# Performance work log

Measured on AMD Instinct MI355X. Metric: run time of the kernel, lower is better.

The kernel has to match this reference:

```python
import jax, jax.numpy as jnp
import numpy as np

N_NODES = 50000
N_EDGES = 800000
D_IN = 128
HC = 128
D_OUT = 128
BN_EPS = 1e-5
RRELU_SLOPE = (1.0 / 8.0 + 1.0 / 3.0) / 2.0  # RReLU eval mode: (lower+upper)/2 = 11/48


def setup_inputs() -> dict:
    key = jax.random.key(0)
    ks = jax.random.split(key, 10)
    s_in = 1.0 / np.sqrt(D_IN)
    s_hc = 1.0 / np.sqrt(HC)
    return {
        "x": jax.random.normal(ks[0], (N_NODES, D_IN), jnp.float32),
        "edge_index": jax.random.randint(ks[1], (2, N_EDGES), 0, N_NODES),
        "edge_attr": jax.random.uniform(ks[2], (N_EDGES,), jnp.float32),
        # conv1: GraphConv(D_IN -> HC): lin_rel (with bias) + lin_root (no bias)
        "W1_rel": jax.random.normal(ks[3], (HC, D_IN), jnp.float32) * s_in,
        "b1": jnp.zeros((HC,), jnp.float32),
        "W1_root": jax.random.normal(ks[4], (HC, D_IN), jnp.float32) * s_in,
        # bn1 affine params
        "gamma": jnp.ones((HC,), jnp.float32),
        "beta": jnp.zeros((HC,), jnp.float32),
        # conv2: GraphConv(HC -> D_OUT)
        "W2_rel": jax.random.normal(ks[5], (D_OUT, HC), jnp.float32) * s_hc,
        "b2": jnp.zeros((D_OUT,), jnp.float32),
        "W2_root": jax.random.normal(ks[6], (D_OUT, HC), jnp.float32) * s_hc,
    }


def graph_conv(x, src, tgt, edge_w, W_rel, b_rel, W_root):
    # message: edge_weight * x[src]; aggregate: scatter-add into target nodes
    msg = x[src] * edge_w[:, None]                                   # [E, F]
    agg = jax.ops.segment_sum(msg, tgt, num_segments=x.shape[0])     # [N, F]
    return agg @ W_rel.T + b_rel + x @ W_root.T                      # [N, F_out]


def reference(x, edge_index, edge_attr, W1_rel, b1, W1_root, gamma, beta, W2_rel, b2, W2_root):
    src, tgt = edge_index[0], edge_index[1]
    h = graph_conv(x, src, tgt, edge_attr, W1_rel, b1, W1_root)      # [N, HC]
    # BatchNorm1d (training mode: biased batch stats over node dim)
    mean = h.mean(axis=0)
    var = h.var(axis=0)
    h = (h - mean) * jax.lax.rsqrt(var + BN_EPS) * gamma + beta
    # RReLU (deterministic eval slope)
    h = jnp.where(h >= 0, h, h * RRELU_SLOPE)
    return graph_conv(h, src, tgt, edge_attr, W2_rel, b2, W2_root)   # [N, D_OUT]
```

## Files before the change

### kernel.cpp

```cpp
#include <hip/hip_runtime.h>

#define N_NODES 50000
#define N_EDGES 800000
#define F 128
#define BN_EPS 1e-5f
#define SLOPE 0.22916666666666666f

#define NBKT 196
#define BKT_CAP 8192
#define P1_CHUNK 4096
#define P1_EPB 16
#define P1_BLKS 196
#define CASTX_BLKS 6250
#define CASTW_BLKS 64
#define BKT_FINAL_CAP 9984
#define REC_CAP 1160192
#define N_RT 3125
#define NPART 8

typedef __attribute__((ext_vector_type(8))) short bf16x8;
typedef __attribute__((ext_vector_type(4))) float f32x4;
typedef unsigned long long u64;

__device__ __forceinline__ float bf2f(ushort u) {
    union { uint i; float f; } v; v.i = (uint)u << 16; return v.f;
}
__device__ __forceinline__ ushort f2bf(float f) {
    union { float f; uint i; } v; v.f = f;
    uint r = v.i + 0x7fffu + ((v.i >> 16) & 1u);
    return (ushort)(r >> 16);
}

__global__ __launch_bounds__(256) void s1p_k(const int* __restrict__ src,
        const int* __restrict__ tgt, const float* __restrict__ ew,
        int* __restrict__ bcur, u64* __restrict__ stg,
        const float* __restrict__ x, ushort* __restrict__ xb,
        const float* __restrict__ W1r, const float* __restrict__ W1t,
        const float* __restrict__ W2r, const float* __restrict__ W2t,
        ushort* __restrict__ wb) {
    const int b = blockIdx.x;
    if (b >= P1_BLKS) {
        if (b < P1_BLKS + CASTX_BLKS) {
            int i = (b - P1_BLKS) * 256 + threadIdx.x;
            float4 v = reinterpret_cast<const float4*>(x)[i];
            ushort4 o;
            o.x = f2bf(v.x); o.y = f2bf(v.y); o.z = f2bf(v.z); o.w = f2bf(v.w);
            reinterpret_cast<ushort4*>(xb)[i] = o;
        } else {
            int i = (b - P1_BLKS - CASTX_BLKS) * 256 + threadIdx.x;
            int m = i >> 12;
            int j = i & 4095;
            const float* sp = (m == 0) ? W1r : (m == 1) ? W1t : (m == 2) ? W2r : W2t;
            float4 v = reinterpret_cast<const float4*>(sp)[j];
            ushort4 o;
            o.x = f2bf(v.x); o.y = f2bf(v.y); o.z = f2bf(v.z); o.w = f2bf(v.w);
            reinterpret_cast<ushort4*>(wb)[i] = o;
        }
        return;
    }
    __shared__ uint cnt[256];
    __shared__ uint base[256];
    __shared__ uint lcur[256];
    __shared__ uint gbase[256];
    __shared__ u64 lrec[P1_CHUNK];

    const int e0 = b * P1_CHUNK;
    const int nE = min(P1_CHUNK, N_EDGES - e0);
    cnt[threadIdx.x] = 0;
    __syncthreads();

    u64 myrec[P1_EPB];
    bool myok[P1_EPB];
#pragma unroll
    for (int k = 0; k < P1_EPB; ++k) {
        int idx = threadIdx.x + (k << 8);
        bool ok = idx < nE;
        myok[k] = ok;
        if (ok) {
            int e = e0 + idx;
            uint t = (uint)tgt[e];
            uint lo = (uint)(ushort)src[e] | ((uint)f2bf(ew[e]) << 16);
            myrec[k] = (u64)lo | ((u64)t << 32);
            atomicAdd(&cnt[t >> 8], 1u);
        }
    }
    __syncthreads();
    uint v = cnt[threadIdx.x];
    base[threadIdx.x] = v;
    __syncthreads();
    for (int o = 1; o < 256; o <<= 1) {
        uint t = (threadIdx.x >= (unsigned)o) ? base[threadIdx.x - o] : 0;
        __syncthreads();
        base[threadIdx.x] += t;
        __syncthreads();
    }
    uint excl = base[threadIdx.x] - v;
    base[threadIdx.x] = excl;
    lcur[threadIdx.x] = excl;
    if (threadIdx.x < NBKT && v > 0)
        gbase[threadIdx.x] = (uint)threadIdx.x * BKT_CAP +
                             (uint)atomicAdd(&bcur[threadIdx.x], (int)v);
    __syncthreads();
#pragma unroll
    for (int k = 0; k < P1_EPB; ++k) {
        if (myok[k]) {
            uint bb = (uint)(myrec[k] >> 40);
            uint slot = atomicAdd(&lcur[bb], 1u);
            lrec[slot] = myrec[k];
        }
    }
    __syncthreads();
    for (int s = threadIdx.x; s < nE; s += 256) {
        u64 r = lrec[s];
        uint bb = (uint)(r >> 40);
        stg[gbase[bb] + ((uint)s - base[bb])] = r;
    }
}

__global__ __launch_bounds__(256) void sort2_k(const int* __restrict__ bcur,
        const u64* __restrict__ stg, uint* __restrict__ recs, int2* __restrict__ rng) {
    __shared__ int lcnt[256];
    __shared__ int lcur[256];
    __shared__ int sc[256];
    __shared__ int fbase_s;
    __shared__ uint lrec[BKT_FINAL_CAP];
    const int b = blockIdx.x;
    const int tid = threadIdx.x;

    int cnt_t = (tid < NBKT) ? bcur[tid] : 0;
    int stride_t = (tid < NBKT) ? (((cnt_t + 7) & ~7) + 1792) : 0;
    sc[tid] = stride_t;
    lcnt[tid] = 0;
    __syncthreads();
    for (int o = 1; o < 256; o <<= 1) {
        int t = (tid >= o) ? sc[tid - o] : 0;
        __syncthreads();
        sc[tid] += t;
        __syncthreads();
    }
    if (tid == b) fbase_s = sc[tid] - stride_t;
    __syncthreads();
    const int fbase = fbase_s;
    const int cnt = bcur[b];
    const u64* sb = stg + (size_t)b * BKT_CAP;

    for (int i = tid; i < cnt; i += 256)
        atomicAdd(&lcnt[(int)(sb[i] >> 32) & 255], 1);
    __syncthreads();
    const int node = b * 256 + tid;
    int myc = lcnt[tid];
    int myp = (myc + 7) & ~7;
    if (node >= N_NODES) myp = 0;
    sc[tid] = myp;
    __syncthreads();
    for (int o = 1; o < 256; o <<= 1) {
        int t = (tid >= o) ? sc[tid - o] : 0;
        __syncthreads();
        sc[tid] += t;
        __syncthreads();
    }
    const int myoff = sc[tid] - myp;
    const int ptot = sc[255];
    lcur[tid] = myoff;
    if (node < N_NODES) rng[node] = make_int2(fbase + myoff, fbase + myoff + myp);
    for (int i = tid; i < ptot; i += 256) lrec[i] = 0;
    __syncthreads();
    for (int i = tid; i < cnt; i += 256) {
        u64 r = sb[i];
        int n = (int)(r >> 32) & 255;
        int p = atomicAdd(&lcur[n], 1);
        lrec[p] = (uint)r;
    }
    __syncthreads();
    for (int i = tid; i < ptot; i += 256) recs[fbase + i] = lrec[i];
}

template <int LAYER>
__global__ __launch_bounds__(256) void fused_k(
        const ushort* __restrict__ featb, const int2* __restrict__ rng,
        const uint* __restrict__ recs, const ushort* __restrict__ Wr,
        const ushort* __restrict__ Wt, const float* __restrict__ bias,
        const float* __restrict__ gamma, const float* __restrict__ beta,
        float* __restrict__ Sp, float* __restrict__ S2p,
        ushort* __restrict__ outh, float* __restrict__ outf) {
    __shared__ __align__(16) uint aggu[16 * 64];
    __shared__ __align__(16) float scs[128];
    __shared__ __align__(16) float shs[128];

    const int tid = threadIdx.x;
    const int lane = tid & 63;
    const int wave = tid >> 6;
    const int row0 = blockIdx.x * 16;

    if (LAYER == 2) {
        if (tid < 128) {
            float s = 0.f, q = 0.f;
#pragma unroll
            for (int p = 0; p < NPART; ++p) {
                s += Sp[p * 128 + tid];
                q += S2p[p * 128 + tid];
            }
            float mean = s * (1.f / N_NODES);
            float var = q * (1.f / N_NODES) - mean * mean;
            float inv = rsqrtf(var + BN_EPS);
            float sc = gamma[tid] * inv;
            scs[tid] = sc;
            shs[tid] = beta[tid] - mean * sc;
        }
        __syncthreads();
    }

    const int lane2 = lane * 2;
    float lsc0 = 1.f, lsh0 = 0.f, lsc1 = 1.f, lsh1 = 0.f;
    if (LAYER == 2) {
        lsc0 = scs[lane2]; lsh0 = shs[lane2];
        lsc1 = scs[lane2 + 1]; lsh1 = shs[lane2 + 1];
    }

#pragma unroll
    for (int i = 0; i < 4; ++i) {
        const int r = wave * 4 + i;
        const int2 rr = rng[row0 + r];
        float a0 = 0.f, a1 = 0.f;
        for (int p = rr.x; p < rr.y; p += 8) {
            uint4 ra = *reinterpret_cast<const uint4*>(recs + p);
            uint4 rb = *reinterpret_cast<const uint4*>(recs + p + 4);
            uint u0 = *reinterpret_cast<const uint*>(featb + (size_t)(ra.x & 0xffffu) * F + lane2);
            uint u1 = *reinterpret_cast<const uint*>(featb + (size_t)(ra.y & 0xffffu) * F + lane2);
            uint u2 = *reinterpret_cast<const uint*>(featb + (size_t)(ra.z & 0xffffu) * F + lane2);
            uint u3 = *reinterpret_cast<const uint*>(featb + (size_t)(ra.w & 0xffffu) * F + lane2);
            uint u4 = *reinterpret_cast<const uint*>(featb + (size_t)(rb.x & 0xffffu) * F + lane2);
            uint u5 = *reinterpret_cast<const uint*>(featb + (size_t)(rb.y & 0xffffu) * F + lane2);
            uint u6 = *reinterpret_cast<const uint*>(featb + (size_t)(rb.z & 0xffffu) * F + lane2);
            uint u7 = *reinterpret_cast<const uint*>(featb + (size_t)(rb.w & 0xffffu) * F + lane2);
            float w0 = bf2f((ushort)(ra.x >> 16)), w1 = bf2f((ushort)(ra.y >> 16));
            float w2 = bf2f((ushort)(ra.z >> 16)), w3 = bf2f((ushort)(ra.w >> 16));
            float w4 = bf2f((ushort)(rb.x >> 16)), w5 = bf2f((ushort)(rb.y >> 16));
            float w6 = bf2f((ushort)(rb.z >> 16)), w7 = bf2f((ushort)(rb.w >> 16));
            auto proc = [&](uint u, float w) {
                float t0 = bf2f((ushort)u);
                float t1 = bf2f((ushort)(u >> 16));
                if (LAYER == 2) {
                    t0 = t0 * lsc0 + lsh0; t0 = fmaxf(t0, t0 * SLOPE);
                    t1 = t1 * lsc1 + lsh1; t1 = fmaxf(t1, t1 * SLOPE);
                }
                a0 += w * t0;
                a1 += w * t1;
            };
            proc(u0, w0); proc(u1, w1); proc(u2, w2); proc(u3, w3);
            proc(u4, w4); proc(u5, w5); proc(u6, w6); proc(u7, w7);
        }
        aggu[(r * 64 + lane) ^ ((r & 7) << 2)] =
            (uint)f2bf(a0) | ((uint)f2bf(a1) << 16);
    }
    __syncthreads();

    const int quad = lane >> 4;
    const int l16 = lane & 15;
    const int cb = wave * 32;
    const float bias0 = bias[cb + l16];
    const float bias1 = bias[cb + 16 + l16];

    f32x4 acc0 = {0.f, 0.f, 0.f, 0.f};
    f32x4 acc1 = {0.f, 0.f, 0.f, 0.f};

#pragma unroll
    for (int s = 0; s < 4; ++s) {
        const int k0 = s * 32 + quad * 8;
        const int ai = (l16 * 64 + (k0 >> 1)) ^ ((l16 & 7) << 2);
        bf16x8 aR = *reinterpret_cast<const bf16x8*>(&aggu[ai]);
        bf16x8 w0 = *reinterpret_cast<const bf16x8*>(Wr + (cb + l16) * F + k0);
        bf16x8 w1 = *reinterpret_cast<const bf16x8*>(Wr + (cb + 16 + l16) * F + k0);
        acc0 = __builtin_amdgcn_mfma_f32_16x16x32_bf16(aR, w0, acc0, 0, 0, 0);
        acc1 = __builtin_amdgcn_mfma_f32_16x16x32_bf16(aR, w1, acc1, 0, 0, 0);
    }
#pragma unroll
    for (int s = 0; s < 4; ++s) {
        const int k0 = s * 32 + quad * 8;
        bf16x8 aT = *reinterpret_cast<const bf16x8*>(featb + (size_t)(row0 + l16) * F + k0);
        if (LAYER == 2) {
#pragma unroll
            for (int e = 0; e < 8; ++e) {
                float t = bf2f((ushort)aT[e]) * scs[k0 + e] + shs[k0 + e];
                t = fmaxf(t, t * SLOPE);
                aT[e] = (short)f2bf(t);
            }
        }
        bf16x8 w0 = *reinterpret_cast<const bf16x8*>(Wt + (cb + l16) * F + k0);
        bf16x8 w1 = *reinterpret_cast<const bf16x8*>(Wt + (cb + 16 + l16) * F + k0);
        acc0 = __builtin_amdgcn_mfma_f32_16x16x32_bf16(aT, w0, acc0, 0, 0, 0);
        acc1 = __builtin_amdgcn_mfma_f32_16x16x32_bf16(aT, w1, acc1, 0, 0, 0);
    }

    const int rbase = row0 + quad * 4;
    if (LAYER == 1) {
        float s0 = 0.f, q0 = 0.f, s1 = 0.f, q1 = 0.f;
#pragma unroll
        for (int g = 0; g < 4; ++g) {
            float v0 = acc0[g] + bias0;
            float v1 = acc1[g] + bias1;
            outh[(size_t)(rbase + g) * F + cb + l16] = f2bf(v0);
            outh[(size_t)(rbase + g) * F + cb + 16 + l16] = f2bf(v1);
            s0 += v0; q0 += v0 * v0;
            s1 += v1; q1 += v1 * v1;
        }
        s0 += __shfl_down(s0, 32); s0 += __shfl_down(s0, 16);
        q0 += __shfl_down(q0, 32); q0 += __shfl_down(q0, 16);
        s1 += __shfl_down(s1, 32); s1 += __shfl_down(s1, 16);
        q1 += __shfl_down(q1, 32); q1 += __shfl_down(q1, 16);
        if (lane < 16) {
            float* Sb = Sp + (size_t)(blockIdx.x & (NPART - 1)) * 128;
            float* S2b = S2p + (size_t)(blockIdx.x & (NPART - 1)) * 128;
            unsafeAtomicAdd(&Sb[cb + lane], s0);
            unsafeAtomicAdd(&S2b[cb + lane], q0);
            unsafeAtomicAdd(&Sb[cb + 16 + lane], s1);
            unsafeAtomicAdd(&S2b[cb + 16 + lane], q1);
        }
    } else {
#pragma unroll
        for (int g = 0; g < 4; ++g) {
            outf[(size_t)(rbase + g) * F + cb + l16] = acc0[g] + bias0;
            outf[(size_t)(rbase + g) * F + cb + 16 + l16] = acc1[g] + bias1;
        }
    }
}

extern "C" void kernel_launch(void* const* d_in, const int* in_sizes, int n_in,
                              void* d_out, int out_size, void* d_ws, size_t ws_size,
                              hipStream_t stream) {
    const float* x     = (const float*)d_in[0];
    const int*   ei    = (const int*)d_in[1];
    const float* ea    = (const float*)d_in[2];
    const float* W1r   = (const float*)d_in[3];
    const float* b1    = (const float*)d_in[4];
    const float* W1t   = (const float*)d_in[5];
    const float* gamma = (const float*)d_in[6];
    const float* beta  = (const float*)d_in[7];
    const float* W2r   = (const float*)d_in[8];
    const float* b2    = (const float*)d_in[9];
    const float* W2t   = (const float*)d_in[10];
    float* out = (float*)d_out;

    char* ws = (char*)d_ws;
    size_t off = 0;
    u64*    stg   = (u64*)(ws + off);    off += (size_t)NBKT * BKT_CAP * 8;
    ushort* featb = (ushort*)(ws + off); off += (size_t)N_NODES * F * 2;
    uint*   recs  = (uint*)(ws + off);   off += (size_t)REC_CAP * 4;
    int*    bcur  = (int*)(ws + off);    off += 256 * 4;
    float*  Sp    = (float*)(ws + off);  off += NPART * 128 * 4;
    float*  S2p   = (float*)(ws + off);  off += NPART * 128 * 4;
    int2*   rng   = (int2*)(ws + off);   off += (size_t)N_NODES * 8;
    ushort* wb    = (ushort*)(ws + off); off += 4 * 16384 * 2;
    ushort* hraw  = (ushort*)stg;

    const int* srcp = ei;
    const int* tgtp = ei + N_EDGES;

    hipMemsetAsync(bcur, 0, 256 * 4 + 2 * NPART * 128 * 4, stream);
    s1p_k<<<P1_BLKS + CASTX_BLKS + CASTW_BLKS, 256, 0, stream>>>(
        srcp, tgtp, ea, bcur, stg, x, featb, W1r, W1t, W2r, W2t, wb);
    sort2_k<<<NBKT, 256, 0, stream>>>(bcur, stg, recs, rng);

    fused_k<1><<<N_RT, 256, 0, stream>>>(featb, rng, recs, wb, wb + 16384, b1,
                                         gamma, beta, Sp, S2p, hraw, out);
    fused_k<2><<<N_RT, 256, 0, stream>>>(hraw, rng, recs, wb + 32768, wb + 49152, b2,
                                         gamma, beta, Sp, S2p, hraw, out);
}
```

Measured before the change: 230.3 us.

## Widen gather to 16-byte row loads and split BN+RReLU into separate pass

The gather loop changes so each lane loads 16 bytes (8 bf16 features) per neighbour instead of 4 bytes. Each quarter-wave handles a different pair of edges, and the partial sums are combined with cross-lane shuffles. Batch-norm and RReLU move out of the layer-2 gather into a standalone elementwise kernel that writes the activated features once. This removes the redundant per-edge normalisation math and the per-block statistics recompute. In exchange it adds an extra kernel launch, a full read and write pass over the hidden features, and shuffle reductions, and it uses v_cvt_pk_bf16_f32 for packing.

Result: slower. 254.8 us (+10.7%).

```diff
diff --git a/kernel.cpp b/kernel.cpp
--- a/kernel.cpp
+++ b/kernel.cpp
@@ -29,6 +29,11 @@
     union { float f; uint i; } v; v.f = f;
     uint r = v.i + 0x7fffu + ((v.i >> 16) & 1u);
     return (ushort)(r >> 16);
+}
+__device__ __forceinline__ uint cvtpk(float lo, float hi) {
+    uint r;
+    asm("v_cvt_pk_bf16_f32 %0, %1, %2" : "=v"(r) : "v"(lo), "v"(hi));
+    return r;
 }
 
 __global__ __launch_bounds__(256) void s1p_k(const int* __restrict__ src,
@@ -175,88 +180,64 @@
     for (int i = tid; i < ptot; i += 256) recs[fbase + i] = lrec[i];
 }
 
+__device__ __forceinline__ void fma8(float* a, uint4 u, float w) {
+    a[0] = fmaf(w, __uint_as_float(u.x << 16), a[0]);
+    a[1] = fmaf(w, __uint_as_float(u.x & 0xffff0000u), a[1]);
+    a[2] = fmaf(w, __uint_as_float(u.y << 16), a[2]);
+    a[3] = fmaf(w, __uint_as_float(u.y & 0xffff0000u), a[3]);
+    a[4] = fmaf(w, __uint_as_float(u.z << 16), a[4]);
+    a[5] = fmaf(w, __uint_as_float(u.z & 0xffff0000u), a[5]);
+    a[6] = fmaf(w, __uint_as_float(u.w << 16), a[6]);
+    a[7] = fmaf(w, __uint_as_float(u.w & 0xffff0000u), a[7]);
+}
+
 template <int LAYER>
 __global__ __launch_bounds__(256) void fused_k(
         const ushort* __restrict__ featb, const int2* __restrict__ rng,
         const uint* __restrict__ recs, const ushort* __restrict__ Wr,
         const ushort* __restrict__ Wt, const float* __restrict__ bias,
-        const float* __restrict__ gamma, const float* __restrict__ beta,
         float* __restrict__ Sp, float* __restrict__ S2p,
         ushort* __restrict__ outh, float* __restrict__ outf) {
     __shared__ __align__(16) uint aggu[16 * 64];
-    __shared__ __align__(16) float scs[128];
-    __shared__ __align__(16) float shs[128];
 
     const int tid = threadIdx.x;
     const int lane = tid & 63;
     const int wave = tid >> 6;
     const int row0 = blockIdx.x * 16;
-
-    if (LAYER == 2) {
-        if (tid < 128) {
-            float s = 0.f, q = 0.f;
-#pragma unroll
-            for (int p = 0; p < NPART; ++p) {
-                s += Sp[p * 128 + tid];
-                q += S2p[p * 128 + tid];
-            }
-            float mean = s * (1.f / N_NODES);
-            float var = q * (1.f / N_NODES) - mean * mean;
-            float inv = rsqrtf(var + BN_EPS);
-            float sc = gamma[tid] * inv;
-            scs[tid] = sc;
-            shs[tid] = beta[tid] - mean * sc;
-        }
-        __syncthreads();
-    }
-
-    const int lane2 = lane * 2;
-    float lsc0 = 1.f, lsh0 = 0.f, lsc1 = 1.f, lsh1 = 0.f;
-    if (LAYER == 2) {
-        lsc0 = scs[lane2]; lsh0 = shs[lane2];
-        lsc1 = scs[lane2 + 1]; lsh1 = shs[lane2 + 1];
-    }
+    const int quad = lane >> 4;
+    const int l16 = lane & 15;
+    const uint fbyte = (uint)l16 << 4;
+    const int qq = quad * 2;
+    const char* fb = (const char*)featb;
 
 #pragma unroll
     for (int i = 0; i < 4; ++i) {
         const int r = wave * 4 + i;
         const int2 rr = rng[row0 + r];
-        float a0 = 0.f, a1 = 0.f;
+        float a[8] = {0.f, 0.f, 0.f, 0.f, 0.f, 0.f, 0.f, 0.f};
         for (int p = rr.x; p < rr.y; p += 8) {
-            uint4 ra = *reinterpret_cast<const uint4*>(recs + p);
-            uint4 rb = *reinterpret_cast<const uint4*>(recs + p + 4);
-            uint u0 = *reinterpret_cast<const uint*>(featb + (size_t)(ra.x & 0xffffu) * F + lane2);
-            uint u1 = *reinterpret_cast<const uint*>(featb + (size_t)(ra.y & 0xffffu) * F + lane2);
-            uint u2 = *reinterpret_cast<const uint*>(featb + (size_t)(ra.z & 0xffffu) * F + lane2);
-            uint u3 = *reinterpret_cast<const uint*>(featb + (size_t)(ra.w & 0xffffu) * F + lane2);
-            uint u4 = *reinterpret_cast<const uint*>(featb + (size_t)(rb.x & 0xffffu) * F + lane2);
-            uint u5 = *reinterpret_cast<const uint*>(featb + (size_t)(rb.y & 0xffffu) * F + lane2);
-            uint u6 = *reinterpret_cast<const uint*>(featb + (size_t)(rb.z & 0xffffu) * F + lane2);
-            uint u7 = *reinterpret_cast<const uint*>(featb + (size_t)(rb.w & 0xffffu) * F + lane2);
-            float w0 = bf2f((ushort)(ra.x >> 16)), w1 = bf2f((ushort)(ra.y >> 16));
-            float w2 = bf2f((ushort)(ra.z >> 16)), w3 = bf2f((ushort)(ra.w >> 16));
-            float w4 = bf2f((ushort)(rb.x >> 16)), w5 = bf2f((ushort)(rb.y >> 16));
-            float w6 = bf2f((ushort)(rb.z >> 16)), w7 = bf2f((ushort)(rb.w >> 16));
-            auto proc = [&](uint u, float w) {
-                float t0 = bf2f((ushort)u);
-                float t1 = bf2f((ushort)(u >> 16));
-                if (LAYER == 2) {
-                    t0 = t0 * lsc0 + lsh0; t0 = fmaxf(t0, t0 * SLOPE);
-                    t1 = t1 * lsc1 + lsh1; t1 = fmaxf(t1, t1 * SLOPE);
-                }
-                a0 += w * t0;
-                a1 += w * t1;
-            };
-            proc(u0, w0); proc(u1, w1); proc(u2, w2); proc(u3, w3);
-            proc(u4, w4); proc(u5, w5); proc(u6, w6); proc(u7, w7);
-        }
-        aggu[(r * 64 + lane) ^ ((r & 7) << 2)] =
-            (uint)f2bf(a0) | ((uint)f2bf(a1) << 16);
-    }
-    __syncthreads();
-
-    const int quad = lane >> 4;
-    const int l16 = lane & 15;
+            uint2 rc = *reinterpret_cast<const uint2*>(recs + p + qq);
+            uint4 u0 = *reinterpret_cast<const uint4*>(fb + (((rc.x & 0xffffu) << 8) + fbyte));
+            uint4 u1 = *reinterpret_cast<const uint4*>(fb + (((rc.y & 0xffffu) << 8) + fbyte));
+            fma8(a, u0, __uint_as_float(rc.x & 0xffff0000u));
+            fma8(a, u1, __uint_as_float(rc.y & 0xffff0000u));
+        }
+#pragma unroll
+        for (int j = 0; j < 8; ++j) {
+            a[j] += __shfl_xor(a[j], 16);
+            a[j] += __shfl_xor(a[j], 32);
+        }
+        uint o0 = cvtpk(a[0], a[1]);
+        uint o1 = cvtpk(a[2], a[3]);
+        uint o2 = cvtpk(a[4], a[5]);
+        uint o3 = cvtpk(a[6], a[7]);
+        if (lane < 16) {
+            const int idx = ((r * 64) + (l16 << 2)) ^ ((r & 7) << 2);
+            *reinterpret_cast<uint4*>(&aggu[idx]) = make_uint4(o0, o1, o2, o3);
+        }
+    }
+    __syncthreads();
+
     const int cb = wave * 32;
     const float bias0 = bias[cb + l16];
     const float bias1 = bias[cb + 16 + l16];
@@ -278,14 +259,6 @@
     for (int s = 0; s < 4; ++s) {
         const int k0 = s * 32 + quad * 8;
         bf16x8 aT = *reinterpret_cast<const bf16x8*>(featb + (size_t)(row0 + l16) * F + k0);
-        if (LAYER == 2) {
-#pragma unroll
-            for (int e = 0; e < 8; ++e) {
-                float t = bf2f((ushort)aT[e]) * scs[k0 + e] + shs[k0 + e];
-                t = fmaxf(t, t * SLOPE);
-                aT[e] = (short)f2bf(t);
-            }
-        }
         bf16x8 w0 = *reinterpret_cast<const bf16x8*>(Wt + (cb + l16) * F + k0);
         bf16x8 w1 = *reinterpret_cast<const bf16x8*>(Wt + (cb + 16 + l16) * F + k0);
         acc0 = __builtin_amdgcn_mfma_f32_16x16x32_bf16(aT, w0, acc0, 0, 0, 0);
@@ -323,6 +296,48 @@
             outf[(size_t)(rbase + g) * F + cb + 16 + l16] = acc1[g] + bias1;
         }
     }
+}
+
+__global__ __launch_bounds__(256) void norm_act_k(const ushort* __restrict__ hraw,
+        const float* __restrict__ Sp, const float* __restrict__ S2p,
+        const float* __restrict__ gamma, const float* __restrict__ beta,
+        ushort* __restrict__ hb) {
+    __shared__ float sc_s[128], sh_s[128];
+    if (threadIdx.x < 128) {
+        int j = threadIdx.x;
+        float s = 0.f, q = 0.f;
+#pragma unroll
+        for (int p = 0; p < NPART; ++p) {
+            s += Sp[p * 128 + j];
+            q += S2p[p * 128 + j];
+        }
+        float mean = s * (1.f / N_NODES);
+        float var = q * (1.f / N_NODES) - mean * mean;
+        float inv = rsqrtf(var + BN_EPS);
+        float sc = gamma[j] * inv;
+        sc_s[j] = sc;
+        sh_s[j] = beta[j] - mean * sc;
+    }
+    __syncthreads();
+    int i = blockIdx.x * 256 + threadIdx.x;
+    int cbase = (i & 31) * 4;
+    uint2 u = reinterpret_cast<const uint2*>(hraw)[i];
+    float4 v = make_float4(bf2f((ushort)u.x), bf2f((ushort)(u.x >> 16)),
+                           bf2f((ushort)u.y), bf2f((ushort)(u.y >> 16)));
+    float4 sc = *reinterpret_cast<const float4*>(&sc_s[cbase]);
+    float4 sh = *reinterpret_cast<const float4*>(&sh_s[cbase]);
+    v.x = v.x * sc.x + sh.x;
+    v.y = v.y * sc.y + sh.y;
+    v.z = v.z * sc.z + sh.z;
+    v.w = v.w * sc.w + sh.w;
+    v.x = v.x >= 0.f ? v.x : v.x * SLOPE;
+    v.y = v.y >= 0.f ? v.y : v.y * SLOPE;
+    v.z = v.z >= 0.f ? v.z : v.z * SLOPE;
+    v.w = v.w >= 0.f ? v.w : v.w * SLOPE;
+    uint2 o;
+    o.x = cvtpk(v.x, v.y);
+    o.y = cvtpk(v.z, v.w);
+    reinterpret_cast<uint2*>(hb)[i] = o;
 }
 
 extern "C" void kernel_launch(void* const* d_in, const int* in_sizes, int n_in,
@@ -362,7 +377,8 @@
     sort2_k<<<NBKT, 256, 0, stream>>>(bcur, stg, recs, rng);
 
     fused_k<1><<<N_RT, 256, 0, stream>>>(featb, rng, recs, wb, wb + 16384, b1,
-                                         gamma, beta, Sp, S2p, hraw, out);
-    fused_k<2><<<N_RT, 256, 0, stream>>>(hraw, rng, recs, wb + 32768, wb + 49152, b2,
-                                         gamma, beta, Sp, S2p, hraw, out);
-}
+                                         Sp, S2p, hraw, out);
+    norm_act_k<<<CASTX_BLKS, 256, 0, stream>>>(hraw, Sp, S2p, gamma, beta, featb);
+    fused_k<2><<<N_RT, 256, 0, stream>>>(featb, rng, recs, wb + 32768, wb + 49152, b2,
+                                         Sp, S2p, hraw, out);
+}
```

## Replace two-pass bucket sort with histogram-scan-atomic scatter CSR build

Applied to the files above, without the earlier changes.

Replaces the staged two-level bucket sort of edges by target with a global-atomic degree histogram, a two-kernel prefix scan producing per-node padded ranges, and a scatter kernel that places each packed edge record using an atomic per-node cursor. This removes the 64-bit staging buffer and its shared-memory sorting passes. In exchange it adds two small launches, a larger memset covering the full record array, and many contended global atomics. Edge order within each node becomes nondeterministic.

Result: slower. 301.4 us (+30.9%).

```diff
diff --git a/kernel.cpp b/kernel.cpp
--- a/kernel.cpp
+++ b/kernel.cpp
@@ -6,14 +6,11 @@
 #define BN_EPS 1e-5f
 #define SLOPE 0.22916666666666666f
 
-#define NBKT 196
-#define BKT_CAP 8192
-#define P1_CHUNK 4096
-#define P1_EPB 16
-#define P1_BLKS 196
 #define CASTX_BLKS 6250
 #define CASTW_BLKS 64
-#define BKT_FINAL_CAP 9984
+#define HIST_BLKS 782
+#define SCAT_BLKS 782
+#define SCAN_BLKS 196
 #define REC_CAP 1160192
 #define N_RT 3125
 #define NPART 8
@@ -30,24 +27,86 @@
     uint r = v.i + 0x7fffu + ((v.i >> 16) & 1u);
     return (ushort)(r >> 16);
 }
-
-__global__ __launch_bounds__(256) void s1p_k(const int* __restrict__ src,
+__device__ __forceinline__ uint cvtpk(float lo, float hi) {
+    uint r;
+    asm("v_cvt_pk_bf16_f32 %0, %1, %2" : "=v"(r) : "v"(lo), "v"(hi));
+    return r;
+}
+
+__global__ __launch_bounds__(256) void hist_k(const int* __restrict__ tgt,
+                                              int* __restrict__ deg) {
+    const int i0 = blockIdx.x * 1024 + threadIdx.x;
+#pragma unroll
+    for (int k = 0; k < 4; ++k) {
+        int i = i0 + (k << 8);
+        if (i < N_EDGES) atomicAdd(&deg[tgt[i]], 1);
+    }
+}
+
+__global__ __launch_bounds__(256) void scan1_k(const int* __restrict__ deg,
+        int* __restrict__ lofs, int* __restrict__ bsum) {
+    __shared__ int sc[256];
+    const int tid = threadIdx.x;
+    const int n = blockIdx.x * 256 + tid;
+    int d = (n < N_NODES) ? deg[n] : 0;
+    int myp = (d + 7) & ~7;
+    sc[tid] = myp;
+    __syncthreads();
+    for (int o = 1; o < 256; o <<= 1) {
+        int t = (tid >= o) ? sc[tid - o] : 0;
+        __syncthreads();
+        sc[tid] += t;
+        __syncthreads();
+    }
+    if (n < N_NODES) lofs[n] = sc[tid] - myp;
+    if (tid == 255) bsum[blockIdx.x] = sc[255];
+}
+
+__global__ __launch_bounds__(256) void fin_k(const int* __restrict__ deg,
+        const int* __restrict__ lofs, const int* __restrict__ bsum,
+        int2* __restrict__ rng, int* __restrict__ cur) {
+    __shared__ int sc[256];
+    const int tid = threadIdx.x;
+    int v = (tid < SCAN_BLKS) ? bsum[tid] : 0;
+    sc[tid] = v;
+    __syncthreads();
+    for (int o = 1; o < 256; o <<= 1) {
+        int t = (tid >= o) ? sc[tid - o] : 0;
+        __syncthreads();
+        sc[tid] += t;
+        __syncthreads();
+    }
+    __shared__ int base_s;
+    if (tid == blockIdx.x) base_s = sc[tid] - v;
+    __syncthreads();
+    const int base = base_s;
+    const int n = blockIdx.x * 256 + tid;
+    if (n < N_NODES) {
+        int d = deg[n];
+        int myp = (d + 7) & ~7;
+        int st = base + lofs[n];
+        rng[n] = make_int2(st, st + myp);
+        cur[n] = st;
+    }
+}
+
+__global__ __launch_bounds__(256) void scat_k(const int* __restrict__ src,
         const int* __restrict__ tgt, const float* __restrict__ ew,
-        int* __restrict__ bcur, u64* __restrict__ stg,
+        int* __restrict__ cur, uint* __restrict__ recs,
         const float* __restrict__ x, ushort* __restrict__ xb,
         const float* __restrict__ W1r, const float* __restrict__ W1t,
         const float* __restrict__ W2r, const float* __restrict__ W2t,
         ushort* __restrict__ wb) {
     const int b = blockIdx.x;
-    if (b >= P1_BLKS) {
-        if (b < P1_BLKS + CASTX_BLKS) {
-            int i = (b - P1_BLKS) * 256 + threadIdx.x;
+    if (b >= SCAT_BLKS) {
+        if (b < SCAT_BLKS + CASTX_BLKS) {
+            int i = (b - SCAT_BLKS) * 256 + threadIdx.x;
             float4 v = reinterpret_cast<const float4*>(x)[i];
             ushort4 o;
             o.x = f2bf(v.x); o.y = f2bf(v.y); o.z = f2bf(v.z); o.w = f2bf(v.w);
             reinterpret_cast<ushort4*>(xb)[i] = o;
         } else {
-            int i = (b - P1_BLKS - CASTX_BLKS) * 256 + threadIdx.x;
+            int i = (b - SCAT_BLKS - CASTX_BLKS) * 256 + threadIdx.x;
             int m = i >> 12;
             int j = i & 4095;
             const float* sp = (m == 0) ? W1r : (m == 1) ? W1t : (m == 2) ? W2r : W2t;
@@ -58,121 +117,16 @@
         }
         return;
     }
-    __shared__ uint cnt[256];
-    __shared__ uint base[256];
-    __shared__ uint lcur[256];
-    __shared__ uint gbase[256];
-    __shared__ u64 lrec[P1_CHUNK];
-
-    const int e0 = b * P1_CHUNK;
-    const int nE = min(P1_CHUNK, N_EDGES - e0);
-    cnt[threadIdx.x] = 0;
-    __syncthreads();
-
-    u64 myrec[P1_EPB];
-    bool myok[P1_EPB];
-#pragma unroll
-    for (int k = 0; k < P1_EPB; ++k) {
-        int idx = threadIdx.x + (k << 8);
-        bool ok = idx < nE;
-        myok[k] = ok;
-        if (ok) {
-            int e = e0 + idx;
-            uint t = (uint)tgt[e];
-            uint lo = (uint)(ushort)src[e] | ((uint)f2bf(ew[e]) << 16);
-            myrec[k] = (u64)lo | ((u64)t << 32);
-            atomicAdd(&cnt[t >> 8], 1u);
-        }
-    }
-    __syncthreads();
-    uint v = cnt[threadIdx.x];
-    base[threadIdx.x] = v;
-    __syncthreads();
-    for (int o = 1; o < 256; o <<= 1) {
-        uint t = (threadIdx.x >= (unsigned)o) ? base[threadIdx.x - o] : 0;
-        __syncthreads();
-        base[threadIdx.x] += t;
-        __syncthreads();
-    }
-    uint excl = base[threadIdx.x] - v;
-    base[threadIdx.x] = excl;
-    lcur[threadIdx.x] = excl;
-    if (threadIdx.x < NBKT && v > 0)
-        gbase[threadIdx.x] = (uint)threadIdx.x * BKT_CAP +
-                             (uint)atomicAdd(&bcur[threadIdx.x], (int)v);
-    __syncthreads();
-#pragma unroll
-    for (int k = 0; k < P1_EPB; ++k) {
-        if (myok[k]) {
-            uint bb = (uint)(myrec[k] >> 40);
-            uint slot = atomicAdd(&lcur[bb], 1u);
-            lrec[slot] = myrec[k];
-        }
-    }
-    __syncthreads();
-    for (int s = threadIdx.x; s < nE; s += 256) {
-        u64 r = lrec[s];
-        uint bb = (uint)(r >> 40);
-        stg[gbase[bb] + ((uint)s - base[bb])] = r;
-    }
-}
-
-__global__ __launch_bounds__(256) void sort2_k(const int* __restrict__ bcur,
-        const u64* __restrict__ stg, uint* __restrict__ recs, int2* __restrict__ rng) {
-    __shared__ int lcnt[256];
-    __shared__ int lcur[256];
-    __shared__ int sc[256];
-    __shared__ int fbase_s;
-    __shared__ uint lrec[BKT_FINAL_CAP];
-    const int b = blockIdx.x;
-    const int tid = threadIdx.x;
-
-    int cnt_t = (tid < NBKT) ? bcur[tid] : 0;
-    int stride_t = (tid < NBKT) ? (((cnt_t + 7) & ~7) + 1792) : 0;
-    sc[tid] = stride_t;
-    lcnt[tid] = 0;
-    __syncthreads();
-    for (int o = 1; o < 256; o <<= 1) {
-        int t = (tid >= o) ? sc[tid - o] : 0;
-        __syncthreads();
-        sc[tid] += t;
-        __syncthreads();
-    }
-    if (tid == b) fbase_s = sc[tid] - stride_t;
-    __syncthreads();
-    const int fbase = fbase_s;
-    const int cnt = bcur[b];
-    const u64* sb = stg + (size_t)b * BKT_CAP;
-
-    for (int i = tid; i < cnt; i += 256)
-        atomicAdd(&lcnt[(int)(sb[i] >> 32) & 255], 1);
-    __syncthreads();
-    const int node = b * 256 + tid;
-    int myc = lcnt[tid];
-    int myp = (myc + 7) & ~7;
-    if (node >= N_NODES) myp = 0;
-    sc[tid] = myp;
-    __syncthreads();
-    for (int o = 1; o < 256; o <<= 1) {
-        int t = (tid >= o) ? sc[tid - o] : 0;
-        __syncthreads();
-        sc[tid] += t;
-        __syncthreads();
-    }
-    const int myoff = sc[tid] - myp;
-    const int ptot = sc[255];
-    lcur[tid] = myoff;
-    if (node < N_NODES) rng[node] = make_int2(fbase + myoff, fbase + myoff + myp);
-    for (int i = tid; i < ptot; i += 256) lrec[i] = 0;
-    __syncthreads();
-    for (int i = tid; i < cnt; i += 256) {
-        u64 r = sb[i];
-        int n = (int)(r >> 32) & 255;
-        int p = atomicAdd(&lcur[n], 1);
-        lrec[p] = (uint)r;
-    }
-    __syncthreads();
-    for (int i = tid; i < ptot; i += 256) recs[fbase + i] = lrec[i];
+    const int i0 = b * 1024 + threadIdx.x;
+#pragma unroll
+    for (int k = 0; k < 4; ++k) {
+        int i = i0 + (k << 8);
+        if (i < N_EDGES) {
+            uint rec = (uint)(ushort)src[i] | ((uint)f2bf(ew[i]) << 16);
+            int pos = atomicAdd(&cur[tgt[i]], 1);
+            recs[pos] = rec;
+        }
+    }
 }
 
 template <int LAYER>
@@ -343,23 +297,29 @@
 
     char* ws = (char*)d_ws;
     size_t off = 0;
-    u64*    stg   = (u64*)(ws + off);    off += (size_t)NBKT * BKT_CAP * 8;
     ushort* featb = (ushort*)(ws + off); off += (size_t)N_NODES * F * 2;
+    ushort* hraw  = (ushort*)(ws + off); off += (size_t)N_NODES * F * 2;
+    int2*   rng   = (int2*)(ws + off);   off += (size_t)N_NODES * 8;
+    int*    cur   = (int*)(ws + off);    off += (size_t)N_NODES * 4;
+    int*    lofs  = (int*)(ws + off);    off += (size_t)N_NODES * 4;
+    int*    bsum  = (int*)(ws + off);    off += 256 * 4;
+    ushort* wb    = (ushort*)(ws + off); off += 4 * 16384 * 2;
+    char*   zbase = ws + off;
     uint*   recs  = (uint*)(ws + off);   off += (size_t)REC_CAP * 4;
-    int*    bcur  = (int*)(ws + off);    off += 256 * 4;
+    int*    deg   = (int*)(ws + off);    off += (size_t)N_NODES * 4;
     float*  Sp    = (float*)(ws + off);  off += NPART * 128 * 4;
     float*  S2p   = (float*)(ws + off);  off += NPART * 128 * 4;
-    int2*   rng   = (int2*)(ws + off);   off += (size_t)N_NODES * 8;
-    ushort* wb    = (ushort*)(ws + off); off += 4 * 16384 * 2;
-    ushort* hraw  = (ushort*)stg;
+    size_t  zlen  = (size_t)(ws + off - zbase);
 
     const int* srcp = ei;
     const int* tgtp = ei + N_EDGES;
 
-    hipMemsetAsync(bcur, 0, 256 * 4 + 2 * NPART * 128 * 4, stream);
-    s1p_k<<<P1_BLKS + CASTX_BLKS + CASTW_BLKS, 256, 0, stream>>>(
-        srcp, tgtp, ea, bcur, stg, x, featb, W1r, W1t, W2r, W2t, wb);
-    sort2_k<<<NBKT, 256, 0, stream>>>(bcur, stg, recs, rng);
+    hipMemsetAsync(zbase, 0, zlen, stream);
+    hist_k<<<HIST_BLKS, 256, 0, stream>>>(tgtp, deg);
+    scan1_k<<<SCAN_BLKS, 256, 0, stream>>>(deg, lofs, bsum);
+    fin_k<<<SCAN_BLKS, 256, 0, stream>>>(deg, lofs, bsum, rng, cur);
+    scat_k<<<SCAT_BLKS + CASTX_BLKS + CASTW_BLKS, 256, 0, stream>>>(
+        srcp, tgtp, ea, cur, recs, x, featb, W1r, W1t, W2r, W2t, wb);
 
     fused_k<1><<<N_RT, 256, 0, stream>>>(featb, rng, recs, wb, wb + 16384, b1,
                                          gamma, beta, Sp, S2p, hraw, out);
```

## Replace global-atomic bucket scatter with per-chunk count matrix and gather-based second pass

Applied to the files above, without the earlier changes.

The first sort pass no longer reserves global bucket space with atomics. Each chunk writes its locally bucket-sorted records contiguously, plus per-bucket counts and offsets into count/offset matrices. The second pass gathers each bucket's slices from all chunks using a prefix sum and binary search, and keeps the records in registers instead of reading staging twice. This also removes the hipMemsetAsync by zeroing the BN partial sums inside sort2_k, at the cost of more scattered gather reads, per-element binary searches, and an 18-entry register array that assumes bucket sizes stay bounded.

After: 233.3 us. No clear change (+1.3%).

```diff
diff --git a/kernel.cpp b/kernel.cpp
--- a/kernel.cpp
+++ b/kernel.cpp
@@ -7,14 +7,14 @@
 #define SLOPE 0.22916666666666666f
 
 #define NBKT 196
-#define BKT_CAP 8192
 #define P1_CHUNK 4096
 #define P1_EPB 16
 #define P1_BLKS 196
 #define CASTX_BLKS 6250
 #define CASTW_BLKS 64
 #define BKT_FINAL_CAP 9984
-#define REC_CAP 1160192
+#define BKT_STRIDE 10240
+#define MYR_CAP 18
 #define N_RT 3125
 #define NPART 8
 
@@ -33,7 +33,7 @@
 
 __global__ __launch_bounds__(256) void s1p_k(const int* __restrict__ src,
         const int* __restrict__ tgt, const float* __restrict__ ew,
-        int* __restrict__ bcur, u64* __restrict__ stg,
+        u64* __restrict__ stg, int* __restrict__ cntM, int* __restrict__ offM,
         const float* __restrict__ x, ushort* __restrict__ xb,
         const float* __restrict__ W1r, const float* __restrict__ W1t,
         const float* __restrict__ W2r, const float* __restrict__ W2t,
@@ -61,7 +61,6 @@
     __shared__ uint cnt[256];
     __shared__ uint base[256];
     __shared__ uint lcur[256];
-    __shared__ uint gbase[256];
     __shared__ u64 lrec[P1_CHUNK];
 
     const int e0 = b * P1_CHUNK;
@@ -95,11 +94,11 @@
         __syncthreads();
     }
     uint excl = base[threadIdx.x] - v;
-    base[threadIdx.x] = excl;
     lcur[threadIdx.x] = excl;
-    if (threadIdx.x < NBKT && v > 0)
-        gbase[threadIdx.x] = (uint)threadIdx.x * BKT_CAP +
-                             (uint)atomicAdd(&bcur[threadIdx.x], (int)v);
+    if (threadIdx.x < NBKT) {
+        cntM[threadIdx.x * NBKT + b] = (int)v;
+        offM[threadIdx.x * NBKT + b] = (int)excl;
+    }
     __syncthreads();
 #pragma unroll
     for (int k = 0; k < P1_EPB; ++k) {
@@ -110,26 +109,32 @@
         }
     }
     __syncthreads();
-    for (int s = threadIdx.x; s < nE; s += 256) {
-        u64 r = lrec[s];
-        uint bb = (uint)(r >> 40);
-        stg[gbase[bb] + ((uint)s - base[bb])] = r;
-    }
-}
-
-__global__ __launch_bounds__(256) void sort2_k(const int* __restrict__ bcur,
-        const u64* __restrict__ stg, uint* __restrict__ recs, int2* __restrict__ rng) {
+    for (int s = threadIdx.x; s < nE; s += 256)
+        stg[(size_t)b * P1_CHUNK + s] = lrec[s];
+}
+
+__global__ __launch_bounds__(256) void sort2_k(const int* __restrict__ cntM,
+        const int* __restrict__ offM, const u64* __restrict__ stg,
+        uint* __restrict__ recs, int2* __restrict__ rng,
+        float* __restrict__ Sp, float* __restrict__ S2p) {
+    __shared__ int soff[256];
+    __shared__ int astart[256];
     __shared__ int lcnt[256];
     __shared__ int lcur[256];
     __shared__ int sc[256];
-    __shared__ int fbase_s;
+    __shared__ int tot_s;
     __shared__ uint lrec[BKT_FINAL_CAP];
-    const int b = blockIdx.x;
+    const int B = blockIdx.x;
     const int tid = threadIdx.x;
 
-    int cnt_t = (tid < NBKT) ? bcur[tid] : 0;
-    int stride_t = (tid < NBKT) ? (((cnt_t + 7) & ~7) + 1792) : 0;
-    sc[tid] = stride_t;
+    if (B < NPART && tid < 128) {
+        Sp[B * 128 + tid] = 0.f;
+        S2p[B * 128 + tid] = 0.f;
+    }
+
+    int c = (tid < NBKT) ? cntM[B * NBKT + tid] : 0;
+    soff[tid] = (tid < NBKT) ? offM[B * NBKT + tid] : 0;
+    sc[tid] = c;
     lcnt[tid] = 0;
     __syncthreads();
     for (int o = 1; o < 256; o <<= 1) {
@@ -138,16 +143,29 @@
         sc[tid] += t;
         __syncthreads();
     }
-    if (tid == b) fbase_s = sc[tid] - stride_t;
-    __syncthreads();
-    const int fbase = fbase_s;
-    const int cnt = bcur[b];
-    const u64* sb = stg + (size_t)b * BKT_CAP;
-
-    for (int i = tid; i < cnt; i += 256)
-        atomicAdd(&lcnt[(int)(sb[i] >> 32) & 255], 1);
-    __syncthreads();
-    const int node = b * 256 + tid;
+    astart[tid] = sc[tid] - c;
+    if (tid == 255) tot_s = sc[255];
+    __syncthreads();
+    const int tot = tot_s;
+
+    u64 myr[MYR_CAP];
+#pragma unroll
+    for (int k = 0; k < MYR_CAP; ++k) {
+        int i = tid + (k << 8);
+        if (i < tot) {
+            int lo = 0, hi = NBKT - 1;
+            while (lo < hi) {
+                int mid = (lo + hi + 1) >> 1;
+                if (astart[mid] <= i) lo = mid; else hi = mid - 1;
+            }
+            int j = i - astart[lo];
+            u64 r = stg[(size_t)lo * P1_CHUNK + soff[lo] + j];
+            myr[k] = r;
+            atomicAdd(&lcnt[(int)(r >> 32) & 255], 1);
+        }
+    }
+    __syncthreads();
+    const int node = B * 256 + tid;
     int myc = lcnt[tid];
     int myp = (myc + 7) & ~7;
     if (node >= N_NODES) myp = 0;
@@ -162,14 +180,19 @@
     const int myoff = sc[tid] - myp;
     const int ptot = sc[255];
     lcur[tid] = myoff;
+    const int fbase = B * BKT_STRIDE;
     if (node < N_NODES) rng[node] = make_int2(fbase + myoff, fbase + myoff + myp);
     for (int i = tid; i < ptot; i += 256) lrec[i] = 0;
     __syncthreads();
-    for (int i = tid; i < cnt; i += 256) {
-        u64 r = sb[i];
-        int n = (int)(r >> 32) & 255;
-        int p = atomicAdd(&lcur[n], 1);
-        lrec[p] = (uint)r;
+#pragma unroll
+    for (int k = 0; k < MYR_CAP; ++k) {
+        int i = tid + (k << 8);
+        if (i < tot) {
+            u64 r = myr[k];
+            int n = (int)(r >> 32) & 255;
+            int p = atomicAdd(&lcur[n], 1);
+            lrec[p] = (uint)r;
+        }
     }
     __syncthreads();
     for (int i = tid; i < ptot; i += 256) recs[fbase + i] = lrec[i];
@@ -343,23 +366,23 @@
 
     char* ws = (char*)d_ws;
     size_t off = 0;
-    u64*    stg   = (u64*)(ws + off);    off += (size_t)NBKT * BKT_CAP * 8;
     ushort* featb = (ushort*)(ws + off); off += (size_t)N_NODES * F * 2;
-    uint*   recs  = (uint*)(ws + off);   off += (size_t)REC_CAP * 4;
-    int*    bcur  = (int*)(ws + off);    off += 256 * 4;
+    ushort* hraw  = (ushort*)(ws + off); off += (size_t)N_NODES * F * 2;
+    u64*    stg   = (u64*)(ws + off);    off += (size_t)P1_BLKS * P1_CHUNK * 8;
+    uint*   recs  = (uint*)(ws + off);   off += (size_t)NBKT * BKT_STRIDE * 4;
+    int*    cntM  = (int*)(ws + off);    off += (size_t)NBKT * NBKT * 4;
+    int*    offM  = (int*)(ws + off);    off += (size_t)NBKT * NBKT * 4;
+    int2*   rng   = (int2*)(ws + off);   off += (size_t)N_NODES * 8;
+    ushort* wb    = (ushort*)(ws + off); off += 4 * 16384 * 2;
     float*  Sp    = (float*)(ws + off);  off += NPART * 128 * 4;
     float*  S2p   = (float*)(ws + off);  off += NPART * 128 * 4;
-    int2*   rng   = (int2*)(ws + off);   off += (size_t)N_NODES * 8;
-    ushort* wb    = (ushort*)(ws + off); off += 4 * 16384 * 2;
-    ushort* hraw  = (ushort*)stg;
 
     const int* srcp = ei;
     const int* tgtp = ei + N_EDGES;
 
-    hipMemsetAsync(bcur, 0, 256 * 4 + 2 * NPART * 128 * 4, stream);
     s1p_k<<<P1_BLKS + CASTX_BLKS + CASTW_BLKS, 256, 0, stream>>>(
-        srcp, tgtp, ea, bcur, stg, x, featb, W1r, W1t, W2r, W2t, wb);
-    sort2_k<<<NBKT, 256, 0, stream>>>(bcur, stg, recs, rng);
+        srcp, tgtp, ea, stg, cntM, offM, x, featb, W1r, W1t, W2r, W2t, wb);
+    sort2_k<<<NBKT, 256, 0, stream>>>(cntM, offM, stg, recs, rng, Sp, S2p);
 
     fused_k<1><<<N_RT, 256, 0, stream>>>(featb, rng, recs, wb, wb + 16384, b1,
                                          gamma, beta, Sp, S2p, hraw, out);
```
